# Optimization experiments

Measured on AMD Instinct MI355X. Metric: run time of the kernel, lower is better.

## Reference

```python
import jax, jax.numpy as jnp
import numpy as np

N = 512
H = 128
L = 4
NUM_RBF = 50
CUTOFF = 5.0
NMOL = 16
OUT = 1


def setup_inputs() -> dict:
    key = jax.random.key(0)
    ks = jax.random.split(key, 12)
    s = lambda f: 1.0 / np.sqrt(f)
    atomic_numbers = jax.random.randint(ks[0], (N,), 0, 100)
    positions = jax.random.normal(ks[1], (N, 3), dtype=jnp.float32) * 2.0
    batch = jnp.sort(jax.random.randint(ks[2], (N,), 0, NMOL))
    return {
        'atomic_numbers': atomic_numbers,
        'positions': positions,
        'batch': batch,
        'embed': jax.random.normal(ks[3], (100, H), dtype=jnp.float32) * 0.1,
        'msg_w1': jax.random.normal(ks[4], (L, H + NUM_RBF + 3, H), dtype=jnp.float32) * s(H + NUM_RBF + 3),
        'msg_b1': jnp.zeros((L, H), jnp.float32),
        'msg_w2': jax.random.normal(ks[5], (L, H, H), dtype=jnp.float32) * s(H),
        'msg_b2': jnp.zeros((L, H), jnp.float32),
        'upd_w1': jax.random.normal(ks[6], (L, 2 * H, H), dtype=jnp.float32) * s(2 * H),
        'upd_b1': jnp.zeros((L, H), jnp.float32),
        'upd_w2': jax.random.normal(ks[7], (L, H, H), dtype=jnp.float32) * s(H),
        'upd_b2': jnp.zeros((L, H), jnp.float32),
        'out_w1': jax.random.normal(ks[8], (H, H // 2), dtype=jnp.float32) * s(H),
        'out_b1': jnp.zeros((H // 2,), jnp.float32),
        'out_w2': jax.random.normal(ks[9], (H // 2, OUT), dtype=jnp.float32) * s(H // 2),
        'out_b2': jnp.zeros((OUT,), jnp.float32),
    }


def _forward(atomic_numbers, positions, batch, embed, msg_w1, msg_b1, msg_w2,
             msg_b2, upd_w1, upd_b1, upd_w2, upd_b2, out_w1, out_b1, out_w2, out_b2):
    x = embed[jnp.clip(atomic_numbers, 0, 99)]                      # [N,H]
    # all-pairs geometry: row i = source, col j = target (matches repeat_interleave/repeat)
    diff = positions[:, None, :] - positions[None, :, :]            # [N,N,3]
    dist = jnp.linalg.norm(diff, axis=-1)                           # [N,N]
    not_self = jnp.arange(N)[:, None] != jnp.arange(N)[None, :]
    valid = (dist < CUTOFF) & not_self                              # [N,N] edge mask
    dirs = diff / jnp.maximum(dist, 1e-8)[..., None]                # [N,N,3]
    # gaussian RBF: centers linspace(0, cutoff, num_rbf), width = cutoff/num_rbf
    centers = jnp.linspace(0.0, CUTOFF, NUM_RBF)
    width = CUTOFF / NUM_RBF
    rbf = jnp.exp(-(dist[..., None] - centers) ** 2 / (2.0 * width ** 2))  # [N,N,50]

    for l in range(L):
        # Linear over concat([x_j, rbf, dirs]) split by input blocks (same math)
        Wx = msg_w1[l, :H]
        Wr = msg_w1[l, H:H + NUM_RBF]
        Wd = msg_w1[l, H + NUM_RBF:]
        pre = (x @ Wx)[:, None, :] \
            + jnp.einsum('ijr,rh->ijh', rbf, Wr) \
            + jnp.einsum('ijd,dh->ijh', dirs, Wd) + msg_b1[l]       # [N,N,H]
        m = jax.nn.silu(pre) @ msg_w2[l] + msg_b2[l]                # [N,N,H]
        m = jnp.where(valid[..., None], m, 0.0)
        aggr = m.sum(axis=0)                                        # scatter-add to target j
        upd_in = jnp.concatenate([x, aggr], axis=-1)                # [N,2H]
        x = x + jax.nn.silu(upd_in @ upd_w1[l] + upd_b1[l]) @ upd_w2[l] + upd_b2[l]

    # per-molecule mean pool
    sums = jax.ops.segment_sum(x, batch, num_segments=NMOL)         # [NMOL,H]
    counts = jax.ops.segment_sum(jnp.ones((N,), x.dtype), batch, num_segments=NMOL)
    pooled = sums / jnp.maximum(counts, 1.0)[:, None]
    return jax.nn.silu(pooled @ out_w1 + out_b1) @ out_w2 + out_b2  # [NMOL,OUT]


def reference(atomic_numbers, positions, batch, embed, msg_w1, msg_b1, msg_w2,
              msg_b2, upd_w1, upd_b1, upd_w2, upd_b2, out_w1, out_b1, out_w2, out_b2):
    return _forward(atomic_numbers, positions, batch, embed, msg_w1, msg_b1, msg_w2,
                    msg_b2, upd_w1, upd_b1, upd_w2, upd_b2, out_w1, out_b1, out_w2, out_b2)
```

## Files before the change

### kernel.cpp

```cpp
#include <hip/hip_runtime.h>
#include <math.h>

#define N 512
#define H 128
#define L 4
#define NUM_RBF 50
#define NMOL 16
#define SUPER 64
#define FSTRIDE 72
#define QSPL 4

typedef __attribute__((ext_vector_type(8))) short short8;
typedef __attribute__((ext_vector_type(4))) float float4v;
typedef __attribute__((ext_vector_type(4))) int int4v;

__device__ __forceinline__ float silu_f(float v) {
    return v / (1.0f + __expf(-v));
}

__device__ __forceinline__ unsigned short f2bf(float f) {
    unsigned int u = __float_as_uint(f);
    unsigned int r = (u + 0x7FFFu + ((u >> 16) & 1u)) >> 16;
    return (unsigned short)r;
}

__global__ __launch_bounds__(256) void k_embed_lin(const int* __restrict__ an,
                                                   const float* __restrict__ embed,
                                                   const float* __restrict__ pos,
                                                   const float* __restrict__ wx,
                                                   const float* __restrict__ b1,
                                                   float* __restrict__ x,
                                                   float* __restrict__ a,
                                                   int* __restrict__ nbr,
                                                   int* __restrict__ ncnt) {
    int j = blockIdx.x;
    int tid = threadIdx.x;
    int lane = tid & 63;
    int wv = tid >> 6;

    __shared__ float xs[H];
    __shared__ int wsum[4];

    float pjx = pos[j * 3 + 0], pjy = pos[j * 3 + 1], pjz = pos[j * 3 + 2];

    float xv = 0.0f;
    if (tid < H) {
        int z = an[j];
        z = min(max(z, 0), 99);
        xv = embed[z * H + tid];
        xs[tid] = xv;
    }

    int total = 0;
#pragma unroll
    for (int r = 0; r < 2; r++) {
        int i = r * 256 + tid;
        float dx = pos[i * 3 + 0] - pjx;
        float dy = pos[i * 3 + 1] - pjy;
        float dz = pos[i * 3 + 2] - pjz;
        float d2 = dx * dx + dy * dy + dz * dz;
        int valid = (d2 < 25.0f) && (i != j);
        unsigned long long m = __ballot(valid);
        int pre = __popcll(m & ((1ull << lane) - 1ull));
        if (lane == 0) wsum[wv] = __popcll(m);
        __syncthreads();
        int wbase = total;
        for (int w = 0; w < 4; w++) {
            if (w < wv) wbase += wsum[w];
        }
        int newtotal = total + wsum[0] + wsum[1] + wsum[2] + wsum[3];
        if (valid) nbr[j * 512 + wbase + pre] = i;
        __syncthreads();
        total = newtotal;
    }
    int padded = (total + 63) & ~63;
    for (int s = total + tid; s < padded; s += 256) nbr[j * 512 + s] = j;
    if (tid == 0) ncnt[j] = total;

    if (tid < H) {
        int h = tid;
        float a0 = b1[h], a1 = 0.f, a2 = 0.f, a3 = 0.f;
#pragma unroll 8
        for (int k = 0; k < H; k += 4) {
            a0 += xs[k]     * wx[(k)     * H + h];
            a1 += xs[k + 1] * wx[(k + 1) * H + h];
            a2 += xs[k + 2] * wx[(k + 2) * H + h];
            a3 += xs[k + 3] * wx[(k + 3) * H + h];
        }
        x[j * H + h] = xv;
        a[j * H + h] = (a0 + a1) + (a2 + a3);
    }
}

__global__ __launch_bounds__(256) void k_msg(const float* __restrict__ a,
                                             const float* __restrict__ pos,
                                             const int* __restrict__ nbr,
                                             const int* __restrict__ ncnt,
                                             const float* __restrict__ wfeat,
                                             float* __restrict__ msum4) {
    int bx = blockIdx.x;
    int j = bx >> 2;
    int q = bx & (QSPL - 1);
    int tid = threadIdx.x;
    int lane = tid & 63;
    int wv = tid >> 6;
    int nn = lane & 15;
    int quad = lane >> 4;

    __shared__ unsigned short F[SUPER * FSTRIDE];
    __shared__ int nidx[SUPER];

    int cnt = ncnt[j];
    float pjx = pos[j * 3 + 0], pjy = pos[j * 3 + 1], pjz = pos[j * 3 + 2];

    int hbase = wv * 32;
    short8 bfrag[2][2];
    for (int c = 0; c < 2; c++) {
        for (int t = 0; t < 2; t++) {
            short8 b;
            int h = hbase + 16 * t + nn;
#pragma unroll
            for (int jj = 0; jj < 8; jj++) {
                int k = c * 32 + quad * 8 + jj;
                float v = (k < NUM_RBF + 3) ? wfeat[k * H + h] : 0.0f;
                b[jj] = (short)f2bf(v);
            }
            bfrag[c][t] = b;
        }
    }

    const float DELTA = 5.0f / 49.0f;
    float pacc0 = 0.0f, pacc1 = 0.0f;

    int S = (cnt + 63) >> 6;
    for (int s = q; s < S; s += QSPL) {
        __syncthreads();
        {
            int il = tid >> 2;
            int kb = (tid & 3) * 16;
            int ni = nbr[j * 512 + s * 64 + il];
            if ((tid & 3) == 0) nidx[il] = ni;
            float dx = pos[ni * 3 + 0] - pjx;
            float dy = pos[ni * 3 + 1] - pjy;
            float dz = pos[ni * 3 + 2] - pjz;
            float d = sqrtf(dx * dx + dy * dy + dz * dz);
            float rinv = 1.0f / fmaxf(d, 1e-8f);
            unsigned short vals[16];
#pragma unroll
            for (int qq = 0; qq < 16; qq++) {
                int k = kb + qq;
                float v;
                if (k < NUM_RBF) {
                    float tt = d - (float)k * DELTA;
                    v = __expf(-50.0f * tt * tt);
                } else if (k == NUM_RBF)     v = dx * rinv;
                else if (k == NUM_RBF + 1)   v = dy * rinv;
                else if (k == NUM_RBF + 2)   v = dz * rinv;
                else                         v = 0.0f;
                vals[qq] = f2bf(v);
            }
            unsigned int* dst = (unsigned int*)&F[il * FSTRIDE + kb];
#pragma unroll
            for (int qq = 0; qq < 8; qq++)
                dst[qq] = (unsigned int)vals[2 * qq] | ((unsigned int)vals[2 * qq + 1] << 16);
        }
        __syncthreads();

#pragma unroll
        for (int it = 0; it < SUPER / 16; it++) {
            int lbase = it * 16 + quad * 4;
            int4v ni4 = *(const int4v*)&nidx[lbase];
            float av0[4], av1[4];
#pragma unroll
            for (int r = 0; r < 4; r++) {
                av0[r] = a[ni4[r] * H + hbase + nn];
                av1[r] = a[ni4[r] * H + hbase + 16 + nn];
            }
            short8 afrag0 = *(const short8*)&F[(it * 16 + nn) * FSTRIDE + 0 * 32 + quad * 8];
            short8 afrag1 = *(const short8*)&F[(it * 16 + nn) * FSTRIDE + 1 * 32 + quad * 8];
            float4v acc0 = {0.0f, 0.0f, 0.0f, 0.0f};
            float4v acc1 = {0.0f, 0.0f, 0.0f, 0.0f};
            acc0 = __builtin_amdgcn_mfma_f32_16x16x32_bf16(afrag0, bfrag[0][0], acc0, 0, 0, 0);
            acc0 = __builtin_amdgcn_mfma_f32_16x16x32_bf16(afrag1, bfrag[1][0], acc0, 0, 0, 0);
            acc1 = __builtin_amdgcn_mfma_f32_16x16x32_bf16(afrag0, bfrag[0][1], acc1, 0, 0, 0);
            acc1 = __builtin_amdgcn_mfma_f32_16x16x32_bf16(afrag1, bfrag[1][1], acc1, 0, 0, 0);
#pragma unroll
            for (int r = 0; r < 4; r++) {
                float vm = (s * 64 + lbase + r < cnt) ? 1.0f : 0.0f;
                pacc0 += vm * silu_f(acc0[r] + av0[r]);
                pacc1 += vm * silu_f(acc1[r] + av1[r]);
            }
        }
    }

    pacc0 += __shfl_xor(pacc0, 16, 64);
    pacc0 += __shfl_xor(pacc0, 32, 64);
    pacc1 += __shfl_xor(pacc1, 16, 64);
    pacc1 += __shfl_xor(pacc1, 32, 64);
    if (lane < 16) {
        msum4[(q * N + j) * H + hbase + nn]      = pacc0;
        msum4[(q * N + j) * H + hbase + 16 + nn] = pacc1;
    }
}

__global__ __launch_bounds__(512) void k_update(const float* __restrict__ msum4,
                                                const int* __restrict__ ncnt,
                                                const float* __restrict__ w2,
                                                const float* __restrict__ b2,
                                                const float* __restrict__ u1,
                                                const float* __restrict__ ub1,
                                                const float* __restrict__ u2,
                                                const float* __restrict__ ub2,
                                                float* __restrict__ x,
                                                const float* __restrict__ wxn,
                                                const float* __restrict__ b1n,
                                                float* __restrict__ a_next) {
    int j = blockIdx.x;
    int h = threadIdx.x & 127;
    int grp = threadIdx.x >> 7;

    __shared__ float sj[H], xj[H], ag[H], hid[H], xn[H];
    __shared__ float part[4][H];

    if (grp == 0) {
        xj[h] = x[j * H + h];
    } else if (grp == 1) {
        sj[h] = msum4[j * H + h] + msum4[(N + j) * H + h]
              + msum4[(2 * N + j) * H + h] + msum4[(3 * N + j) * H + h];
    }
    int c = ncnt[j];
    __syncthreads();

    {
        float p0 = 0.f, p1 = 0.f, p2 = 0.f, p3 = 0.f;
        int k0 = grp * 32;
#pragma unroll 8
        for (int k = 0; k < 32; k += 4) {
            p0 += sj[k0 + k]     * w2[(k0 + k)     * H + h];
            p1 += sj[k0 + k + 1] * w2[(k0 + k + 1) * H + h];
            p2 += sj[k0 + k + 2] * w2[(k0 + k + 2) * H + h];
            p3 += sj[k0 + k + 3] * w2[(k0 + k + 3) * H + h];
        }
        part[grp][h] = (p0 + p1) + (p2 + p3);
    }
    __syncthreads();
    if (grp == 0) ag[h] = part[0][h] + part[1][h] + part[2][h] + part[3][h] + (float)c * b2[h];
    __syncthreads();

    {
        const float* src = (grp < 2) ? xj : ag;
        int sbase = (grp & 1) * 64;
        int k0 = grp * 64;
        float p0 = 0.f, p1 = 0.f, p2 = 0.f, p3 = 0.f;
#pragma unroll 8
        for (int k = 0; k < 64; k += 4) {
            p0 += src[sbase + k]     * u1[(k0 + k)     * H + h];
            p1 += src[sbase + k + 1] * u1[(k0 + k + 1) * H + h];
            p2 += src[sbase + k + 2] * u1[(k0 + k + 2) * H + h];
            p3 += src[sbase + k + 3] * u1[(k0 + k + 3) * H + h];
        }
        part[grp][h] = (p0 + p1) + (p2 + p3);
    }
    __syncthreads();
    if (grp == 0) hid[h] = silu_f(part[0][h] + part[1][h] + part[2][h] + part[3][h] + ub1[h]);
    __syncthreads();

    {
        float p0 = 0.f, p1 = 0.f, p2 = 0.f, p3 = 0.f;
        int k0 = grp * 32;
#pragma unroll 8
        for (int k = 0; k < 32; k += 4) {
            p0 += hid[k0 + k]     * u2[(k0 + k)     * H + h];
            p1 += hid[k0 + k + 1] * u2[(k0 + k + 1) * H + h];
            p2 += hid[k0 + k + 2] * u2[(k0 + k + 2) * H + h];
            p3 += hid[k0 + k + 3] * u2[(k0 + k + 3) * H + h];
        }
        part[grp][h] = (p0 + p1) + (p2 + p3);
    }
    __syncthreads();
    if (grp == 0) {
        float xv = xj[h] + part[0][h] + part[1][h] + part[2][h] + part[3][h] + ub2[h];
        x[j * H + h] = xv;
        xn[h] = xv;
    }

    if (a_next != nullptr) {
        __syncthreads();
        float p0 = 0.f, p1 = 0.f, p2 = 0.f, p3 = 0.f;
        int k0 = grp * 32;
#pragma unroll 8
        for (int k = 0; k < 32; k += 4) {
            p0 += xn[k0 + k]     * wxn[(k0 + k)     * H + h];
            p1 += xn[k0 + k + 1] * wxn[(k0 + k + 1) * H + h];
            p2 += xn[k0 + k + 2] * wxn[(k0 + k + 2) * H + h];
            p3 += xn[k0 + k + 3] * wxn[(k0 + k + 3) * H + h];
        }
        part[grp][h] = (p0 + p1) + (p2 + p3);
        __syncthreads();
        if (grp == 0)
            a_next[j * H + h] = part[0][h] + part[1][h] + part[2][h] + part[3][h] + b1n[h];
    }
}

__global__ __launch_bounds__(H) void k_pool(const float* __restrict__ x,
                                            const int* __restrict__ batch,
                                            const float* __restrict__ ow1,
                                            const float* __restrict__ ob1,
                                            const float* __restrict__ ow2,
                                            const float* __restrict__ ob2,
                                            float* __restrict__ out) {
    int m = blockIdx.x;
    int h = threadIdx.x;
    __shared__ int lo_s, hi_s;
    __shared__ float pooled[H];
    __shared__ float hid[H / 2];

    if (h == 0) {
        int a = 0, b = N;
        while (a < b) { int mid = (a + b) >> 1; if (batch[mid] < m) a = mid + 1; else b = mid; }
        lo_s = a;
        b = N;
        while (a < b) { int mid = (a + b) >> 1; if (batch[mid] < m + 1) a = mid + 1; else b = mid; }
        hi_s = a;
    }
    __syncthreads();

    int lo = lo_s, hi = hi_s;
    float s = 0.0f;
    for (int i = lo; i < hi; i++) s += x[i * H + h];
    pooled[h] = s / (float)max(hi - lo, 1);
    __syncthreads();

    if (h < H / 2) {
        float p0 = 0.f, p1 = 0.f;
        for (int k = 0; k < H; k += 2) {
            p0 += pooled[k]     * ow1[(k)     * (H / 2) + h];
            p1 += pooled[k + 1] * ow1[(k + 1) * (H / 2) + h];
        }
        hid[h] = silu_f(p0 + p1 + ob1[h]);
    }
    __syncthreads();

    if (h == 0) {
        float o = ob2[0];
        for (int k = 0; k < H / 2; k++) o += hid[k] * ow2[k];
        out[m] = o;
    }
}

extern "C" void kernel_launch(void* const* d_in, const int* in_sizes, int n_in,
                              void* d_out, int out_size, void* d_ws, size_t ws_size,
                              hipStream_t stream) {
    const int*   an      = (const int*)d_in[0];
    const float* pos     = (const float*)d_in[1];
    const int*   batch   = (const int*)d_in[2];
    const float* embed   = (const float*)d_in[3];
    const float* msg_w1  = (const float*)d_in[4];
    const float* msg_b1  = (const float*)d_in[5];
    const float* msg_w2  = (const float*)d_in[6];
    const float* msg_b2  = (const float*)d_in[7];
    const float* upd_w1  = (const float*)d_in[8];
    const float* upd_b1  = (const float*)d_in[9];
    const float* upd_w2  = (const float*)d_in[10];
    const float* upd_b2  = (const float*)d_in[11];
    const float* out_w1  = (const float*)d_in[12];
    const float* out_b1  = (const float*)d_in[13];
    const float* out_w2  = (const float*)d_in[14];
    const float* out_b2  = (const float*)d_in[15];
    float* out = (float*)d_out;

    float* x     = (float*)d_ws;
    float* a     = x + N * H;
    float* msum4 = a + N * H;
    int*   nbr   = (int*)(msum4 + QSPL * N * H);
    int*   ncnt  = nbr + N * 512;

    const int W1ROWS = H + NUM_RBF + 3;

    k_embed_lin<<<N, 256, 0, stream>>>(an, embed, pos, msg_w1, msg_b1, x, a, nbr, ncnt);
    for (int l = 0; l < L; l++) {
        k_msg<<<QSPL * N, 256, 0, stream>>>(a, pos, nbr, ncnt,
                                            msg_w1 + l * W1ROWS * H + H * H, msum4);
        const float* wxn = (l + 1 < L) ? (msg_w1 + (l + 1) * W1ROWS * H) : nullptr;
        const float* b1n = (l + 1 < L) ? (msg_b1 + (l + 1) * H) : nullptr;
        float* an_ = (l + 1 < L) ? a : nullptr;
        k_update<<<N, 512, 0, stream>>>(msum4, ncnt,
                                        msg_w2 + l * H * H, msg_b2 + l * H,
                                        upd_w1 + l * 2 * H * H, upd_b1 + l * H,
                                        upd_w2 + l * H * H, upd_b2 + l * H, x,
                                        wxn, b1n, an_);
    }
    k_pool<<<NMOL, H, 0, stream>>>(x, batch, out_w1, out_b1, out_w2, out_b2, out);
}
```

Before: 245.4 us.

## Fuse message and update kernels into a single per-node layer kernel

Merges the per-layer message kernel and the update MLP kernel into one block per target atom. The partial message sums stay in shared memory instead of going through a global buffer, and one launch per layer is removed. The per-node neighbor split across four blocks is dropped, so each block walks all neighbor tiles serially with fewer total blocks. The activation buffer is double-buffered so that writing the next layer's input does not race with other blocks reading the current one.

```diff
diff --git a/kernel.cpp b/kernel.cpp
--- a/kernel.cpp
+++ b/kernel.cpp
@@ -8,7 +8,6 @@
 #define NMOL 16
 #define SUPER 64
 #define FSTRIDE 72
-#define QSPL 4
 
 typedef __attribute__((ext_vector_type(8))) short short8;
 typedef __attribute__((ext_vector_type(4))) float float4v;
@@ -92,28 +91,37 @@
     }
 }
 
-__global__ __launch_bounds__(256) void k_msg(const float* __restrict__ a,
-                                             const float* __restrict__ pos,
-                                             const int* __restrict__ nbr,
-                                             const int* __restrict__ ncnt,
-                                             const float* __restrict__ wfeat,
-                                             float* __restrict__ msum4) {
-    int bx = blockIdx.x;
-    int j = bx >> 2;
-    int q = bx & (QSPL - 1);
+__global__ __launch_bounds__(256) void k_layer(const float* __restrict__ a,
+                                               const float* __restrict__ pos,
+                                               const int* __restrict__ nbr,
+                                               const int* __restrict__ ncnt,
+                                               const float* __restrict__ wfeat,
+                                               const float* __restrict__ w2,
+                                               const float* __restrict__ b2,
+                                               const float* __restrict__ u1,
+                                               const float* __restrict__ ub1,
+                                               const float* __restrict__ u2,
+                                               const float* __restrict__ ub2,
+                                               float* __restrict__ x,
+                                               const float* __restrict__ wxn,
+                                               const float* __restrict__ b1n,
+                                               float* __restrict__ a_next) {
+    int j = blockIdx.x;
     int tid = threadIdx.x;
     int lane = tid & 63;
     int wv = tid >> 6;
     int nn = lane & 15;
     int quad = lane >> 4;
+    int hbase = wv * 32;
 
     __shared__ unsigned short F[SUPER * FSTRIDE];
     __shared__ int nidx[SUPER];
+    __shared__ float sj[H], xj[H], ag[H], hid[H], xn[H];
+    __shared__ float part[2][H];
 
     int cnt = ncnt[j];
     float pjx = pos[j * 3 + 0], pjy = pos[j * 3 + 1], pjz = pos[j * 3 + 2];
 
-    int hbase = wv * 32;
     short8 bfrag[2][2];
     for (int c = 0; c < 2; c++) {
         for (int t = 0; t < 2; t++) {
@@ -133,7 +141,7 @@
     float pacc0 = 0.0f, pacc1 = 0.0f;
 
     int S = (cnt + 63) >> 6;
-    for (int s = q; s < S; s += QSPL) {
+    for (int s = 0; s < S; s++) {
         __syncthreads();
         {
             int il = tid >> 2;
@@ -198,107 +206,53 @@
     pacc1 += __shfl_xor(pacc1, 16, 64);
     pacc1 += __shfl_xor(pacc1, 32, 64);
     if (lane < 16) {
-        msum4[(q * N + j) * H + hbase + nn]      = pacc0;
-        msum4[(q * N + j) * H + hbase + 16 + nn] = pacc1;
-    }
-}
-
-__global__ __launch_bounds__(512) void k_update(const float* __restrict__ msum4,
-                                                const int* __restrict__ ncnt,
-                                                const float* __restrict__ w2,
-                                                const float* __restrict__ b2,
-                                                const float* __restrict__ u1,
-                                                const float* __restrict__ ub1,
-                                                const float* __restrict__ u2,
-                                                const float* __restrict__ ub2,
-                                                float* __restrict__ x,
-                                                const float* __restrict__ wxn,
-                                                const float* __restrict__ b1n,
-                                                float* __restrict__ a_next) {
-    int j = blockIdx.x;
-    int h = threadIdx.x & 127;
-    int grp = threadIdx.x >> 7;
-
-    __shared__ float sj[H], xj[H], ag[H], hid[H], xn[H];
-    __shared__ float part[4][H];
-
-    if (grp == 0) {
-        xj[h] = x[j * H + h];
-    } else if (grp == 1) {
-        sj[h] = msum4[j * H + h] + msum4[(N + j) * H + h]
-              + msum4[(2 * N + j) * H + h] + msum4[(3 * N + j) * H + h];
-    }
-    int c = ncnt[j];
+        sj[hbase + nn]      = pacc0;
+        sj[hbase + 16 + nn] = pacc1;
+    }
+    if (tid < H) xj[tid] = x[j * H + tid];
+    __syncthreads();
+
+    int h = tid & 127;
+    int half = tid >> 7;
+
+    float p = 0.0f;
+#pragma unroll 8
+    for (int k = half * 64; k < half * 64 + 64; k++) p += sj[k] * w2[k * H + h];
+    part[half][h] = p;
+    __syncthreads();
+    if (half == 0) ag[h] = part[0][h] + part[1][h] + (float)cnt * b2[h];
     __syncthreads();
 
     {
-        float p0 = 0.f, p1 = 0.f, p2 = 0.f, p3 = 0.f;
-        int k0 = grp * 32;
-#pragma unroll 8
-        for (int k = 0; k < 32; k += 4) {
-            p0 += sj[k0 + k]     * w2[(k0 + k)     * H + h];
-            p1 += sj[k0 + k + 1] * w2[(k0 + k + 1) * H + h];
-            p2 += sj[k0 + k + 2] * w2[(k0 + k + 2) * H + h];
-            p3 += sj[k0 + k + 3] * w2[(k0 + k + 3) * H + h];
-        }
-        part[grp][h] = (p0 + p1) + (p2 + p3);
-    }
-    __syncthreads();
-    if (grp == 0) ag[h] = part[0][h] + part[1][h] + part[2][h] + part[3][h] + (float)c * b2[h];
-    __syncthreads();
-
-    {
-        const float* src = (grp < 2) ? xj : ag;
-        int sbase = (grp & 1) * 64;
-        int k0 = grp * 64;
-        float p0 = 0.f, p1 = 0.f, p2 = 0.f, p3 = 0.f;
-#pragma unroll 8
-        for (int k = 0; k < 64; k += 4) {
-            p0 += src[sbase + k]     * u1[(k0 + k)     * H + h];
-            p1 += src[sbase + k + 1] * u1[(k0 + k + 1) * H + h];
-            p2 += src[sbase + k + 2] * u1[(k0 + k + 2) * H + h];
-            p3 += src[sbase + k + 3] * u1[(k0 + k + 3) * H + h];
-        }
-        part[grp][h] = (p0 + p1) + (p2 + p3);
-    }
-    __syncthreads();
-    if (grp == 0) hid[h] = silu_f(part[0][h] + part[1][h] + part[2][h] + part[3][h] + ub1[h]);
-    __syncthreads();
-
-    {
-        float p0 = 0.f, p1 = 0.f, p2 = 0.f, p3 = 0.f;
-        int k0 = grp * 32;
-#pragma unroll 8
-        for (int k = 0; k < 32; k += 4) {
-            p0 += hid[k0 + k]     * u2[(k0 + k)     * H + h];
-            p1 += hid[k0 + k + 1] * u2[(k0 + k + 1) * H + h];
-            p2 += hid[k0 + k + 2] * u2[(k0 + k + 2) * H + h];
-            p3 += hid[k0 + k + 3] * u2[(k0 + k + 3) * H + h];
-        }
-        part[grp][h] = (p0 + p1) + (p2 + p3);
-    }
-    __syncthreads();
-    if (grp == 0) {
-        float xv = xj[h] + part[0][h] + part[1][h] + part[2][h] + part[3][h] + ub2[h];
+        const float* src = (half == 0) ? xj : ag;
+        p = 0.0f;
+#pragma unroll 8
+        for (int k = 0; k < H; k++) p += src[k] * u1[(half * H + k) * H + h];
+        part[half][h] = p;
+    }
+    __syncthreads();
+    if (half == 0) hid[h] = silu_f(part[0][h] + part[1][h] + ub1[h]);
+    __syncthreads();
+
+    p = 0.0f;
+#pragma unroll 8
+    for (int k = half * 64; k < half * 64 + 64; k++) p += hid[k] * u2[k * H + h];
+    part[half][h] = p;
+    __syncthreads();
+    if (half == 0) {
+        float xv = xj[h] + part[0][h] + part[1][h] + ub2[h];
         x[j * H + h] = xv;
         xn[h] = xv;
     }
 
     if (a_next != nullptr) {
         __syncthreads();
-        float p0 = 0.f, p1 = 0.f, p2 = 0.f, p3 = 0.f;
-        int k0 = grp * 32;
-#pragma unroll 8
-        for (int k = 0; k < 32; k += 4) {
-            p0 += xn[k0 + k]     * wxn[(k0 + k)     * H + h];
-            p1 += xn[k0 + k + 1] * wxn[(k0 + k + 1) * H + h];
-            p2 += xn[k0 + k + 2] * wxn[(k0 + k + 2) * H + h];
-            p3 += xn[k0 + k + 3] * wxn[(k0 + k + 3) * H + h];
-        }
-        part[grp][h] = (p0 + p1) + (p2 + p3);
-        __syncthreads();
-        if (grp == 0)
-            a_next[j * H + h] = part[0][h] + part[1][h] + part[2][h] + part[3][h] + b1n[h];
+        p = 0.0f;
+#pragma unroll 8
+        for (int k = half * 64; k < half * 64 + 64; k++) p += xn[k] * wxn[k * H + h];
+        part[half][h] = p;
+        __syncthreads();
+        if (half == 0) a_next[j * H + h] = part[0][h] + part[1][h] + b1n[h];
     }
 }
 
@@ -369,26 +323,26 @@
     const float* out_b2  = (const float*)d_in[15];
     float* out = (float*)d_out;
 
-    float* x     = (float*)d_ws;
-    float* a     = x + N * H;
-    float* msum4 = a + N * H;
-    int*   nbr   = (int*)(msum4 + QSPL * N * H);
-    int*   ncnt  = nbr + N * 512;
+    float* x    = (float*)d_ws;
+    float* a0   = x + N * H;
+    float* a1   = a0 + N * H;
+    int*   nbr  = (int*)(a1 + N * H);
+    int*   ncnt = nbr + N * 512;
 
     const int W1ROWS = H + NUM_RBF + 3;
 
-    k_embed_lin<<<N, 256, 0, stream>>>(an, embed, pos, msg_w1, msg_b1, x, a, nbr, ncnt);
+    k_embed_lin<<<N, 256, 0, stream>>>(an, embed, pos, msg_w1, msg_b1, x, a0, nbr, ncnt);
     for (int l = 0; l < L; l++) {
-        k_msg<<<QSPL * N, 256, 0, stream>>>(a, pos, nbr, ncnt,
-                                            msg_w1 + l * W1ROWS * H + H * H, msum4);
+        float* a_cur  = (l & 1) ? a1 : a0;
+        float* a_next = (l + 1 < L) ? ((l & 1) ? a0 : a1) : nullptr;
         const float* wxn = (l + 1 < L) ? (msg_w1 + (l + 1) * W1ROWS * H) : nullptr;
         const float* b1n = (l + 1 < L) ? (msg_b1 + (l + 1) * H) : nullptr;
-        float* an_ = (l + 1 < L) ? a : nullptr;
-        k_update<<<N, 512, 0, stream>>>(msum4, ncnt,
-                                        msg_w2 + l * H * H, msg_b2 + l * H,
-                                        upd_w1 + l * 2 * H * H, upd_b1 + l * H,
-                                        upd_w2 + l * H * H, upd_b2 + l * H, x,
-                                        wxn, b1n, an_);
+        k_layer<<<N, 256, 0, stream>>>(a_cur, pos, nbr, ncnt,
+                                       msg_w1 + l * W1ROWS * H + H * H,
+                                       msg_w2 + l * H * H, msg_b2 + l * H,
+                                       upd_w1 + l * 2 * H * H, upd_b1 + l * H,
+                                       upd_w2 + l * H * H, upd_b2 + l * H,
+                                       x, wxn, b1n, a_next);
     }
     k_pool<<<NMOL, H, 0, stream>>>(x, batch, out_w1, out_b1, out_w2, out_b2, out);
 }
```

Measured after the change: 246.9 us. No clear change (+0.6%).

## Fuse message and update kernels into one per-layer kernel with ping-pong activations

Applied to the files above, without the earlier changes.

Merges the per-target message kernel and the node update kernel into a single 512-thread block per atom. Two 256-thread groups each handle alternate 64-neighbour chunks and reduce their sums through shared memory, replacing the four-way split across blocks and the global partial-sum buffer. The precomputed activation buffer is double-buffered so the next layer's values can be written without clobbering ones other blocks still read. This removes one launch per layer and the global round trip, but cuts grid parallelism from 2048 to 512 blocks and makes the fused work sit behind the neighbour loop.

```diff
diff --git a/kernel.cpp b/kernel.cpp
--- a/kernel.cpp
+++ b/kernel.cpp
@@ -8,7 +8,6 @@
 #define NMOL 16
 #define SUPER 64
 #define FSTRIDE 72
-#define QSPL 4
 
 typedef __attribute__((ext_vector_type(8))) short short8;
 typedef __attribute__((ext_vector_type(4))) float float4v;
@@ -92,28 +91,42 @@
     }
 }
 
-__global__ __launch_bounds__(256) void k_msg(const float* __restrict__ a,
-                                             const float* __restrict__ pos,
-                                             const int* __restrict__ nbr,
-                                             const int* __restrict__ ncnt,
-                                             const float* __restrict__ wfeat,
-                                             float* __restrict__ msum4) {
-    int bx = blockIdx.x;
-    int j = bx >> 2;
-    int q = bx & (QSPL - 1);
+__global__ __launch_bounds__(512) void k_layer(const float* __restrict__ a,
+                                               const float* __restrict__ pos,
+                                               const int* __restrict__ nbr,
+                                               const int* __restrict__ ncnt,
+                                               const float* __restrict__ wfeat,
+                                               const float* __restrict__ w2,
+                                               const float* __restrict__ b2,
+                                               const float* __restrict__ u1,
+                                               const float* __restrict__ ub1,
+                                               const float* __restrict__ u2,
+                                               const float* __restrict__ ub2,
+                                               float* __restrict__ x,
+                                               const float* __restrict__ wxn,
+                                               const float* __restrict__ b1n,
+                                               float* __restrict__ a_next) {
+    int j = blockIdx.x;
     int tid = threadIdx.x;
+    int g = tid >> 8;
+    int t8 = tid & 255;
     int lane = tid & 63;
-    int wv = tid >> 6;
+    int wv4 = (tid >> 6) & 3;
     int nn = lane & 15;
     int quad = lane >> 4;
-
-    __shared__ unsigned short F[SUPER * FSTRIDE];
-    __shared__ int nidx[SUPER];
+    int hbase = wv4 * 32;
+
+    __shared__ unsigned short F[2][SUPER * FSTRIDE];
+    __shared__ int nidx[2][SUPER];
+    __shared__ float sjp[2][H];
+    __shared__ float sj[H], xj[H], ag[H], hid[H], xn[H];
+    __shared__ float part[4][H];
 
     int cnt = ncnt[j];
     float pjx = pos[j * 3 + 0], pjy = pos[j * 3 + 1], pjz = pos[j * 3 + 2];
 
-    int hbase = wv * 32;
+    if (tid < 2 * H) sjp[tid >> 7][tid & 127] = 0.0f;
+
     short8 bfrag[2][2];
     for (int c = 0; c < 2; c++) {
         for (int t = 0; t < 2; t++) {
@@ -133,13 +146,15 @@
     float pacc0 = 0.0f, pacc1 = 0.0f;
 
     int S = (cnt + 63) >> 6;
-    for (int s = q; s < S; s += QSPL) {
-        __syncthreads();
-        {
-            int il = tid >> 2;
-            int kb = (tid & 3) * 16;
+    int rounds = (S + 1) >> 1;
+    for (int r = 0; r < rounds; r++) {
+        int s = 2 * r + g;
+        __syncthreads();
+        if (s < S) {
+            int il = t8 >> 2;
+            int kb = (t8 & 3) * 16;
             int ni = nbr[j * 512 + s * 64 + il];
-            if ((tid & 3) == 0) nidx[il] = ni;
+            if ((t8 & 3) == 0) nidx[g][il] = ni;
             float dx = pos[ni * 3 + 0] - pjx;
             float dy = pos[ni * 3 + 1] - pjy;
             float dz = pos[ni * 3 + 2] - pjz;
@@ -159,36 +174,37 @@
                 else                         v = 0.0f;
                 vals[qq] = f2bf(v);
             }
-            unsigned int* dst = (unsigned int*)&F[il * FSTRIDE + kb];
+            unsigned int* dst = (unsigned int*)&F[g][il * FSTRIDE + kb];
 #pragma unroll
             for (int qq = 0; qq < 8; qq++)
                 dst[qq] = (unsigned int)vals[2 * qq] | ((unsigned int)vals[2 * qq + 1] << 16);
         }
         __syncthreads();
-
-#pragma unroll
-        for (int it = 0; it < SUPER / 16; it++) {
-            int lbase = it * 16 + quad * 4;
-            int4v ni4 = *(const int4v*)&nidx[lbase];
-            float av0[4], av1[4];
-#pragma unroll
-            for (int r = 0; r < 4; r++) {
-                av0[r] = a[ni4[r] * H + hbase + nn];
-                av1[r] = a[ni4[r] * H + hbase + 16 + nn];
-            }
-            short8 afrag0 = *(const short8*)&F[(it * 16 + nn) * FSTRIDE + 0 * 32 + quad * 8];
-            short8 afrag1 = *(const short8*)&F[(it * 16 + nn) * FSTRIDE + 1 * 32 + quad * 8];
-            float4v acc0 = {0.0f, 0.0f, 0.0f, 0.0f};
-            float4v acc1 = {0.0f, 0.0f, 0.0f, 0.0f};
-            acc0 = __builtin_amdgcn_mfma_f32_16x16x32_bf16(afrag0, bfrag[0][0], acc0, 0, 0, 0);
-            acc0 = __builtin_amdgcn_mfma_f32_16x16x32_bf16(afrag1, bfrag[1][0], acc0, 0, 0, 0);
-            acc1 = __builtin_amdgcn_mfma_f32_16x16x32_bf16(afrag0, bfrag[0][1], acc1, 0, 0, 0);
-            acc1 = __builtin_amdgcn_mfma_f32_16x16x32_bf16(afrag1, bfrag[1][1], acc1, 0, 0, 0);
-#pragma unroll
-            for (int r = 0; r < 4; r++) {
-                float vm = (s * 64 + lbase + r < cnt) ? 1.0f : 0.0f;
-                pacc0 += vm * silu_f(acc0[r] + av0[r]);
-                pacc1 += vm * silu_f(acc1[r] + av1[r]);
+        if (s < S) {
+#pragma unroll
+            for (int it = 0; it < SUPER / 16; it++) {
+                int lbase = it * 16 + quad * 4;
+                int4v ni4 = *(const int4v*)&nidx[g][lbase];
+                float av0[4], av1[4];
+#pragma unroll
+                for (int rr = 0; rr < 4; rr++) {
+                    av0[rr] = a[ni4[rr] * H + hbase + nn];
+                    av1[rr] = a[ni4[rr] * H + hbase + 16 + nn];
+                }
+                short8 afrag0 = *(const short8*)&F[g][(it * 16 + nn) * FSTRIDE + 0 * 32 + quad * 8];
+                short8 afrag1 = *(const short8*)&F[g][(it * 16 + nn) * FSTRIDE + 1 * 32 + quad * 8];
+                float4v acc0 = {0.0f, 0.0f, 0.0f, 0.0f};
+                float4v acc1 = {0.0f, 0.0f, 0.0f, 0.0f};
+                acc0 = __builtin_amdgcn_mfma_f32_16x16x32_bf16(afrag0, bfrag[0][0], acc0, 0, 0, 0);
+                acc0 = __builtin_amdgcn_mfma_f32_16x16x32_bf16(afrag1, bfrag[1][0], acc0, 0, 0, 0);
+                acc1 = __builtin_amdgcn_mfma_f32_16x16x32_bf16(afrag0, bfrag[0][1], acc1, 0, 0, 0);
+                acc1 = __builtin_amdgcn_mfma_f32_16x16x32_bf16(afrag1, bfrag[1][1], acc1, 0, 0, 0);
+#pragma unroll
+                for (int rr = 0; rr < 4; rr++) {
+                    float vm = (s * 64 + lbase + rr < cnt) ? 1.0f : 0.0f;
+                    pacc0 += vm * silu_f(acc0[rr] + av0[rr]);
+                    pacc1 += vm * silu_f(acc1[rr] + av1[rr]);
+                }
             }
         }
     }
@@ -198,38 +214,16 @@
     pacc1 += __shfl_xor(pacc1, 16, 64);
     pacc1 += __shfl_xor(pacc1, 32, 64);
     if (lane < 16) {
-        msum4[(q * N + j) * H + hbase + nn]      = pacc0;
-        msum4[(q * N + j) * H + hbase + 16 + nn] = pacc1;
-    }
-}
-
-__global__ __launch_bounds__(512) void k_update(const float* __restrict__ msum4,
-                                                const int* __restrict__ ncnt,
-                                                const float* __restrict__ w2,
-                                                const float* __restrict__ b2,
-                                                const float* __restrict__ u1,
-                                                const float* __restrict__ ub1,
-                                                const float* __restrict__ u2,
-                                                const float* __restrict__ ub2,
-                                                float* __restrict__ x,
-                                                const float* __restrict__ wxn,
-                                                const float* __restrict__ b1n,
-                                                float* __restrict__ a_next) {
-    int j = blockIdx.x;
-    int h = threadIdx.x & 127;
-    int grp = threadIdx.x >> 7;
-
-    __shared__ float sj[H], xj[H], ag[H], hid[H], xn[H];
-    __shared__ float part[4][H];
-
-    if (grp == 0) {
-        xj[h] = x[j * H + h];
-    } else if (grp == 1) {
-        sj[h] = msum4[j * H + h] + msum4[(N + j) * H + h]
-              + msum4[(2 * N + j) * H + h] + msum4[(3 * N + j) * H + h];
-    }
-    int c = ncnt[j];
-    __syncthreads();
+        sjp[g][hbase + nn]      = pacc0;
+        sjp[g][hbase + 16 + nn] = pacc1;
+    }
+    if (tid < H) xj[tid] = x[j * H + tid];
+    __syncthreads();
+    if (tid < H) sj[tid] = sjp[0][tid] + sjp[1][tid];
+    __syncthreads();
+
+    int h = tid & 127;
+    int grp = tid >> 7;
 
     {
         float p0 = 0.f, p1 = 0.f, p2 = 0.f, p3 = 0.f;
@@ -244,7 +238,7 @@
         part[grp][h] = (p0 + p1) + (p2 + p3);
     }
     __syncthreads();
-    if (grp == 0) ag[h] = part[0][h] + part[1][h] + part[2][h] + part[3][h] + (float)c * b2[h];
+    if (grp == 0) ag[h] = part[0][h] + part[1][h] + part[2][h] + part[3][h] + (float)cnt * b2[h];
     __syncthreads();
 
     {
@@ -369,26 +363,26 @@
     const float* out_b2  = (const float*)d_in[15];
     float* out = (float*)d_out;
 
-    float* x     = (float*)d_ws;
-    float* a     = x + N * H;
-    float* msum4 = a + N * H;
-    int*   nbr   = (int*)(msum4 + QSPL * N * H);
-    int*   ncnt  = nbr + N * 512;
+    float* x    = (float*)d_ws;
+    float* a0   = x + N * H;
+    float* a1   = a0 + N * H;
+    int*   nbr  = (int*)(a1 + N * H);
+    int*   ncnt = nbr + N * 512;
 
     const int W1ROWS = H + NUM_RBF + 3;
 
-    k_embed_lin<<<N, 256, 0, stream>>>(an, embed, pos, msg_w1, msg_b1, x, a, nbr, ncnt);
+    k_embed_lin<<<N, 256, 0, stream>>>(an, embed, pos, msg_w1, msg_b1, x, a0, nbr, ncnt);
     for (int l = 0; l < L; l++) {
-        k_msg<<<QSPL * N, 256, 0, stream>>>(a, pos, nbr, ncnt,
-                                            msg_w1 + l * W1ROWS * H + H * H, msum4);
+        float* a_cur  = (l & 1) ? a1 : a0;
+        float* a_next = (l + 1 < L) ? ((l & 1) ? a0 : a1) : nullptr;
         const float* wxn = (l + 1 < L) ? (msg_w1 + (l + 1) * W1ROWS * H) : nullptr;
         const float* b1n = (l + 1 < L) ? (msg_b1 + (l + 1) * H) : nullptr;
-        float* an_ = (l + 1 < L) ? a : nullptr;
-        k_update<<<N, 512, 0, stream>>>(msum4, ncnt,
-                                        msg_w2 + l * H * H, msg_b2 + l * H,
-                                        upd_w1 + l * 2 * H * H, upd_b1 + l * H,
-                                        upd_w2 + l * H * H, upd_b2 + l * H, x,
-                                        wxn, b1n, an_);
+        k_layer<<<N, 512, 0, stream>>>(a_cur, pos, nbr, ncnt,
+                                       msg_w1 + l * W1ROWS * H + H * H,
+                                       msg_w2 + l * H * H, msg_b2 + l * H,
+                                       upd_w1 + l * 2 * H * H, upd_b1 + l * H,
+                                       upd_w2 + l * H * H, upd_b2 + l * H,
+                                       x, wxn, b1n, a_next);
     }
     k_pool<<<NMOL, H, 0, stream>>>(x, batch, out_w1, out_b1, out_w2, out_b2, out);
 }
```

After: 230.1 us. -6.3%, faster.
